# Kernel optimization log

Hardware: AMD Instinct MI355X
Metric: run time of the kernel (lower is better)

The kernel has to match this reference:

```python
import jax, jax.numpy as jnp
import numpy as np

N, C, D = 32768, 2048, 512

def setup_inputs() -> dict:
    key = jax.random.key(0)
    k1, k2, k3 = jax.random.split(key, 3)
    X = jax.random.normal(k1, (N, D), dtype=jnp.float32)
    muK = jax.random.normal(k2, (C, D), dtype=jnp.float32)
    # counts per class; zeros mark 'unvisited' classes exercising the masking path
    cK = jax.random.randint(k3, (C,), 0, 3).astype(jnp.float32)
    return {"X": X, "muK": muK, "cK": cK}

def reference(X, muK, cK):
    # find_dists(A=muK, B=X): dist[i, j] = sum_d (muK[j, d] - X[i, d])**2, scores = -dist
    # avoids materializing the N x C x D broadcast intermediate of the original).
    x2 = jnp.sum(X * X, axis=1, keepdims=True)          # (N, 1)
    m2 = jnp.sum(muK * muK, axis=1)                     # (C,)
    scores = -(x2 + m2[None, :] - 2.0 * (X @ muK.T))    # (N, C)
    # unvisited classes (cK == 0) get per-row min score minus 1
    min_col = jnp.min(scores, axis=1, keepdims=True) - 1.0  # (N, 1)
    scores = jnp.where((cK == 0.0)[None, :], min_col, scores)
    # predict(..., return_probas=True) as used in evaluate_
    return jax.nn.softmax(scores, axis=1)
```

## Files before the change

### kernel.cpp

```cpp
#include <hip/hip_runtime.h>
#include <cfloat>

#define N_ROWS 32768
#define N_CLS  2048
#define DIM    512

typedef __attribute__((ext_vector_type(8))) short short8;
typedef __attribute__((ext_vector_type(4))) short short4v;
typedef __attribute__((ext_vector_type(4))) float f32x4;

__device__ __forceinline__ unsigned f2bf_bits(float x) {
    union { float f; unsigned u; } a; a.f = x;
    return (a.u + 0x7fffu + ((a.u >> 16) & 1u)) >> 16;
}
__device__ __forceinline__ float bf_to_f(unsigned bits) {
    union { unsigned u; float f; } a; a.u = bits << 16;
    return a.f;
}
__device__ __forceinline__ void split_bf(float x, short &h, short &l) {
    unsigned hb = f2bf_bits(x);
    h = (short)hb;
    float r = x - bf_to_f(hb);
    l = (short)f2bf_bits(r);
}

__global__ __launch_bounds__(256) void split_kernel(const float* __restrict__ src,
                                                    short* __restrict__ hi,
                                                    short* __restrict__ lo) {
    int idx = blockIdx.x * 256 + threadIdx.x;
    float4 v = ((const float4*)src)[idx];
    short h0, h1, h2, h3, l0, l1, l2, l3;
    split_bf(v.x, h0, l0); split_bf(v.y, h1, l1);
    split_bf(v.z, h2, l2); split_bf(v.w, h3, l3);
    ((short4v*)hi)[idx] = (short4v){h0, h1, h2, h3};
    ((short4v*)lo)[idx] = (short4v){l0, l1, l2, l3};
}

__global__ __launch_bounds__(256) void m2_kernel(const float* __restrict__ muK,
                                                 float* __restrict__ m2) {
    const int j = blockIdx.x;
    const int t = threadIdx.x;
    const float* r = muK + (size_t)j * DIM;
    float a = r[t], b = r[t + 256];
    float s = a * a + b * b;
    for (int off = 32; off; off >>= 1) s += __shfl_xor(s, off);
    __shared__ float sw[4];
    if ((t & 63) == 0) sw[t >> 6] = s;
    __syncthreads();
    if (t == 0) m2[j] = sw[0] + sw[1] + sw[2] + sw[3];
}

#define GLDS16(g, l) __builtin_amdgcn_global_load_lds( \
    (const __attribute__((address_space(1))) unsigned int*)(g), \
    (__attribute__((address_space(3))) unsigned int*)(l), 16, 0, 0)

__global__ __launch_bounds__(256) void gemm_kernel(const short* __restrict__ Xh,
                                                   const short* __restrict__ Xl,
                                                   const short* __restrict__ Mh,
                                                   const short* __restrict__ Ml,
                                                   const float* __restrict__ m2,
                                                   float* __restrict__ S) {
    __shared__ __align__(16) short Ash[128 * 32];
    __shared__ __align__(16) short Asl[128 * 32];
    __shared__ __align__(16) short Bsh[128 * 32];
    __shared__ __align__(16) short Bsl[128 * 32];

    const int tid  = threadIdx.x;
    const int n0   = blockIdx.x * 128;
    const int m0   = blockIdx.y * 128;
    const int w    = tid >> 6;
    const int lane = tid & 63;
    const int wm   = (w >> 1) * 64;
    const int wn   = (w & 1) * 64;
    const int l16  = lane & 15;
    const int quad = lane >> 4;

    const int c0 = w * 128 + lane;
    const int c1 = c0 + 64;
    const size_t ga0 = (size_t)(m0 + (c0 >> 2)) * DIM + (size_t)(((c0 & 3) ^ ((c0 >> 3) & 3)) * 8);
    const size_t ga1 = (size_t)(m0 + (c1 >> 2)) * DIM + (size_t)(((c1 & 3) ^ ((c1 >> 3) & 3)) * 8);
    const size_t gb0 = (size_t)(n0 + (c0 >> 2)) * DIM + (size_t)(((c0 & 3) ^ ((c0 >> 3) & 3)) * 8);
    const size_t gb1 = (size_t)(n0 + (c1 >> 2)) * DIM + (size_t)(((c1 & 3) ^ ((c1 >> 3) & 3)) * 8);

    const int sw = (quad ^ ((l16 >> 1) & 3)) * 8;

    f32x4 acc[4][4];
#pragma unroll
    for (int mt = 0; mt < 4; ++mt)
#pragma unroll
        for (int nt = 0; nt < 4; ++nt)
            acc[mt][nt] = (f32x4){0.f, 0.f, 0.f, 0.f};

#pragma unroll 1
    for (int kt2 = 0; kt2 < 16; ++kt2) {
        const int kk = kt2 * 32;
        __syncthreads();
        GLDS16(Xh + ga0 + kk, &Ash[c0 * 8]);
        GLDS16(Xh + ga1 + kk, &Ash[c1 * 8]);
        GLDS16(Xl + ga0 + kk, &Asl[c0 * 8]);
        GLDS16(Xl + ga1 + kk, &Asl[c1 * 8]);
        GLDS16(Mh + gb0 + kk, &Bsh[c0 * 8]);
        GLDS16(Mh + gb1 + kk, &Bsh[c1 * 8]);
        GLDS16(Ml + gb0 + kk, &Bsl[c0 * 8]);
        GLDS16(Ml + gb1 + kk, &Bsl[c1 * 8]);
        __syncthreads();

        short8 ah[4], al[4];
#pragma unroll
        for (int mt = 0; mt < 4; ++mt) {
            const int ro = (wm + mt * 16 + l16) * 32 + sw;
            ah[mt] = *(const short8*)&Ash[ro];
            al[mt] = *(const short8*)&Asl[ro];
        }
#pragma unroll
        for (int nt = 0; nt < 4; ++nt) {
            const int ro = (wn + nt * 16 + l16) * 32 + sw;
            short8 bh = *(const short8*)&Bsh[ro];
            short8 bl = *(const short8*)&Bsl[ro];
#pragma unroll
            for (int mt = 0; mt < 4; ++mt)
                acc[mt][nt] = __builtin_amdgcn_mfma_f32_16x16x32_bf16(ah[mt], bh, acc[mt][nt], 0, 0, 0);
#pragma unroll
            for (int mt = 0; mt < 4; ++mt)
                acc[mt][nt] = __builtin_amdgcn_mfma_f32_16x16x32_bf16(ah[mt], bl, acc[mt][nt], 0, 0, 0);
#pragma unroll
            for (int mt = 0; mt < 4; ++mt)
                acc[mt][nt] = __builtin_amdgcn_mfma_f32_16x16x32_bf16(al[mt], bh, acc[mt][nt], 0, 0, 0);
        }
    }

#pragma unroll
    for (int nt = 0; nt < 4; ++nt) {
        int col = n0 + wn + nt * 16 + l16;
        float mm = m2[col];
#pragma unroll
        for (int mt = 0; mt < 4; ++mt) {
            int rbase = m0 + wm + mt * 16 + quad * 4;
#pragma unroll
            for (int r = 0; r < 4; ++r)
                S[(size_t)(rbase + r) * N_CLS + col] = 2.0f * acc[mt][nt][r] - mm;
        }
    }
}

#define LDR 40
__global__ __launch_bounds__(256) void gemm_fallback(const float* __restrict__ X,
                                                     const float* __restrict__ muK,
                                                     const float* __restrict__ m2,
                                                     float* __restrict__ S) {
    __shared__ __align__(16) short Ah[128 * LDR];
    __shared__ __align__(16) short Al[128 * LDR];
    __shared__ __align__(16) short Bh[128 * LDR];
    __shared__ __align__(16) short Bl[128 * LDR];
    const int tid  = threadIdx.x;
    const int n0   = blockIdx.x * 128;
    const int m0   = blockIdx.y * 128;
    const int w    = tid >> 6;
    const int lane = tid & 63;
    const int wm   = (w >> 1) * 64;
    const int wn   = (w & 1) * 64;
    const int l16  = lane & 15;
    const int quad = lane >> 4;
    f32x4 acc[4][4];
#pragma unroll
    for (int mt = 0; mt < 4; ++mt)
#pragma unroll
        for (int nt = 0; nt < 4; ++nt)
            acc[mt][nt] = (f32x4){0.f, 0.f, 0.f, 0.f};
    for (int kt = 0; kt < DIM; kt += 32) {
        __syncthreads();
#pragma unroll
        for (int i = 0; i < 4; ++i) {
            int idx = tid + 256 * i;
            int row = idx >> 3;
            int c4  = (idx & 7) * 4;
            float4 fa = *(const float4*)(X + (size_t)(m0 + row) * DIM + kt + c4);
            float4 fb = *(const float4*)(muK + (size_t)(n0 + row) * DIM + kt + c4);
            short h0, h1, h2, h3, l0, l1, l2, l3;
            split_bf(fa.x, h0, l0); split_bf(fa.y, h1, l1);
            split_bf(fa.z, h2, l2); split_bf(fa.w, h3, l3);
            *(short4v*)&Ah[row * LDR + c4] = (short4v){h0, h1, h2, h3};
            *(short4v*)&Al[row * LDR + c4] = (short4v){l0, l1, l2, l3};
            split_bf(fb.x, h0, l0); split_bf(fb.y, h1, l1);
            split_bf(fb.z, h2, l2); split_bf(fb.w, h3, l3);
            *(short4v*)&Bh[row * LDR + c4] = (short4v){h0, h1, h2, h3};
            *(short4v*)&Bl[row * LDR + c4] = (short4v){l0, l1, l2, l3};
        }
        __syncthreads();
        short8 ah[4], al[4];
#pragma unroll
        for (int mt = 0; mt < 4; ++mt) {
            int r = wm + mt * 16 + l16;
            ah[mt] = *(const short8*)&Ah[r * LDR + quad * 8];
            al[mt] = *(const short8*)&Al[r * LDR + quad * 8];
        }
#pragma unroll
        for (int nt = 0; nt < 4; ++nt) {
            int r = wn + nt * 16 + l16;
            short8 bh = *(const short8*)&Bh[r * LDR + quad * 8];
            short8 bl = *(const short8*)&Bl[r * LDR + quad * 8];
#pragma unroll
            for (int mt = 0; mt < 4; ++mt)
                acc[mt][nt] = __builtin_amdgcn_mfma_f32_16x16x32_bf16(ah[mt], bh, acc[mt][nt], 0, 0, 0);
#pragma unroll
            for (int mt = 0; mt < 4; ++mt)
                acc[mt][nt] = __builtin_amdgcn_mfma_f32_16x16x32_bf16(ah[mt], bl, acc[mt][nt], 0, 0, 0);
#pragma unroll
            for (int mt = 0; mt < 4; ++mt)
                acc[mt][nt] = __builtin_amdgcn_mfma_f32_16x16x32_bf16(al[mt], bh, acc[mt][nt], 0, 0, 0);
        }
    }
#pragma unroll
    for (int nt = 0; nt < 4; ++nt) {
        int col = n0 + wn + nt * 16 + l16;
        float mm = m2[col];
#pragma unroll
        for (int mt = 0; mt < 4; ++mt) {
            int rbase = m0 + wm + mt * 16 + quad * 4;
#pragma unroll
            for (int r = 0; r < 4; ++r)
                S[(size_t)(rbase + r) * N_CLS + col] = 2.0f * acc[mt][nt][r] - mm;
        }
    }
}

__device__ __forceinline__ void sm_load_row(float* S, int row, int lane, f32x4* v) {
    const f32x4* pi = (const f32x4*)(S + (size_t)row * N_CLS);
#pragma unroll
    for (int i = 0; i < 8; ++i) v[i] = pi[i * 64 + lane];
}

__device__ __forceinline__ void sm_compute_store(float* S, int row, int lane,
                                                 unsigned msk, f32x4* v) {
    float mn = FLT_MAX, mx = -FLT_MAX;
#pragma unroll
    for (int i = 0; i < 8; ++i) {
        f32x4 s = v[i];
        mn = fminf(mn, fminf(fminf(s.x, s.y), fminf(s.z, s.w)));
        if (!((msk >> (i * 4 + 0)) & 1u)) mx = fmaxf(mx, s.x);
        if (!((msk >> (i * 4 + 1)) & 1u)) mx = fmaxf(mx, s.y);
        if (!((msk >> (i * 4 + 2)) & 1u)) mx = fmaxf(mx, s.z);
        if (!((msk >> (i * 4 + 3)) & 1u)) mx = fmaxf(mx, s.w);
    }
    for (int off = 32; off; off >>= 1) {
        mn = fminf(mn, __shfl_xor(mn, off));
        mx = fmaxf(mx, __shfl_xor(mx, off));
    }
    if (mx == -FLT_MAX) mx = mn - 1.0f;
    const float fill = mn - 1.0f;

    float sum = 0.f;
#pragma unroll
    for (int i = 0; i < 8; ++i) {
        f32x4 s = v[i];
        s.x = __expf(((msk >> (i * 4 + 0)) & 1u ? fill : s.x) - mx);
        s.y = __expf(((msk >> (i * 4 + 1)) & 1u ? fill : s.y) - mx);
        s.z = __expf(((msk >> (i * 4 + 2)) & 1u ? fill : s.z) - mx);
        s.w = __expf(((msk >> (i * 4 + 3)) & 1u ? fill : s.w) - mx);
        sum += s.x + s.y + s.z + s.w;
        v[i] = s;
    }
    for (int off = 32; off; off >>= 1) sum += __shfl_xor(sum, off);
    const float inv = 1.0f / sum;
    f32x4* po = (f32x4*)(S + (size_t)row * N_CLS);
#pragma unroll
    for (int i = 0; i < 8; ++i) {
        f32x4 s = v[i] * inv;
        __builtin_nontemporal_store(s, &po[i * 64 + lane]);
    }
}

__global__ __launch_bounds__(256) void softmax_kernel(float* __restrict__ S,
                                                      const float* __restrict__ cK) {
    const int w    = threadIdx.x >> 6;
    const int lane = threadIdx.x & 63;
    const float4* ck4 = (const float4*)cK;

    unsigned msk = 0;
#pragma unroll
    for (int i = 0; i < 8; ++i) {
        float4 k = ck4[i * 64 + lane];
        if (k.x == 0.f) msk |= 1u << (i * 4 + 0);
        if (k.y == 0.f) msk |= 1u << (i * 4 + 1);
        if (k.z == 0.f) msk |= 1u << (i * 4 + 2);
        if (k.w == 0.f) msk |= 1u << (i * 4 + 3);
    }

    const int r0 = blockIdx.x * 16 + w * 4;
    f32x4 va[8], vb[8];

    sm_load_row(S, r0 + 0, lane, va);
    sm_load_row(S, r0 + 1, lane, vb);
    sm_compute_store(S, r0 + 0, lane, msk, va);
    sm_load_row(S, r0 + 2, lane, va);
    sm_compute_store(S, r0 + 1, lane, msk, vb);
    sm_load_row(S, r0 + 3, lane, vb);
    sm_compute_store(S, r0 + 2, lane, msk, va);
    sm_compute_store(S, r0 + 3, lane, msk, vb);
}

extern "C" void kernel_launch(void* const* d_in, const int* in_sizes, int n_in,
                              void* d_out, int out_size, void* d_ws, size_t ws_size,
                              hipStream_t stream) {
    const float* X   = (const float*)d_in[0];
    const float* muK = (const float*)d_in[1];
    const float* cK  = (const float*)d_in[2];
    float* out = (float*)d_out;

    const size_t XN = (size_t)N_ROWS * DIM;
    const size_t MN = (size_t)N_CLS * DIM;
    const size_t need = (2 * XN + 2 * MN) * sizeof(short) + N_CLS * sizeof(float);

    dim3 grid(N_CLS / 128, N_ROWS / 128);

    if (ws_size >= need) {
        short* Xh = (short*)d_ws;
        short* Xl = Xh + XN;
        short* Mh = Xl + XN;
        short* Ml = Mh + MN;
        float* m2 = (float*)(Ml + MN);
        split_kernel<<<(int)(XN / 4 / 256), 256, 0, stream>>>(X, Xh, Xl);
        split_kernel<<<(int)(MN / 4 / 256), 256, 0, stream>>>(muK, Mh, Ml);
        m2_kernel<<<N_CLS, 256, 0, stream>>>(muK, m2);
        gemm_kernel<<<grid, 256, 0, stream>>>(Xh, Xl, Mh, Ml, m2, out);
    } else {
        float* m2f = (float*)d_ws;
        m2_kernel<<<N_CLS, 256, 0, stream>>>(muK, m2f);
        gemm_fallback<<<grid, 256, 0, stream>>>(X, muK, m2f, out);
    }
    softmax_kernel<<<N_ROWS / 16, 256, 0, stream>>>(out, cK);
}
```

Baseline: 587.4 us.

## Double-buffer LDS tiles to overlap global loads with MFMA compute

The GEMM kernel's shared-memory tiles for the split bf16 hi/lo operands become two buffers each. The loads for the next K-slice are issued into the alternate buffer before the current slice's MFMAs run, and a sched_barrier keeps the compiler from reordering them. This replaces the two barriers per iteration with one at the end of the loop and hides load latency behind compute. In exchange, LDS per block doubles to 64KB, which can lower the number of resident blocks per CU.

After: 584.9 us. About the same (-0.4%).

```diff
diff --git a/kernel.cpp b/kernel.cpp
--- a/kernel.cpp
+++ b/kernel.cpp
@@ -60,10 +60,10 @@
                                                    const short* __restrict__ Ml,
                                                    const float* __restrict__ m2,
                                                    float* __restrict__ S) {
-    __shared__ __align__(16) short Ash[128 * 32];
-    __shared__ __align__(16) short Asl[128 * 32];
-    __shared__ __align__(16) short Bsh[128 * 32];
-    __shared__ __align__(16) short Bsl[128 * 32];
+    __shared__ __align__(16) short Ash[2][128 * 32];
+    __shared__ __align__(16) short Asl[2][128 * 32];
+    __shared__ __align__(16) short Bsh[2][128 * 32];
+    __shared__ __align__(16) short Bsl[2][128 * 32];
 
     const int tid  = threadIdx.x;
     const int n0   = blockIdx.x * 128;
@@ -84,6 +84,17 @@
 
     const int sw = (quad ^ ((l16 >> 1) & 3)) * 8;
 
+#define STAGE(B, KK) do { \
+        GLDS16(Xh + ga0 + (KK), &Ash[B][c0 * 8]); \
+        GLDS16(Xh + ga1 + (KK), &Ash[B][c1 * 8]); \
+        GLDS16(Xl + ga0 + (KK), &Asl[B][c0 * 8]); \
+        GLDS16(Xl + ga1 + (KK), &Asl[B][c1 * 8]); \
+        GLDS16(Mh + gb0 + (KK), &Bsh[B][c0 * 8]); \
+        GLDS16(Mh + gb1 + (KK), &Bsh[B][c1 * 8]); \
+        GLDS16(Ml + gb0 + (KK), &Bsl[B][c0 * 8]); \
+        GLDS16(Ml + gb1 + (KK), &Bsl[B][c1 * 8]); \
+    } while (0)
+
     f32x4 acc[4][4];
 #pragma unroll
     for (int mt = 0; mt < 4; ++mt)
@@ -91,32 +102,27 @@
         for (int nt = 0; nt < 4; ++nt)
             acc[mt][nt] = (f32x4){0.f, 0.f, 0.f, 0.f};
 
+    STAGE(0, 0);
+    __syncthreads();
+
 #pragma unroll 1
     for (int kt2 = 0; kt2 < 16; ++kt2) {
-        const int kk = kt2 * 32;
-        __syncthreads();
-        GLDS16(Xh + ga0 + kk, &Ash[c0 * 8]);
-        GLDS16(Xh + ga1 + kk, &Ash[c1 * 8]);
-        GLDS16(Xl + ga0 + kk, &Asl[c0 * 8]);
-        GLDS16(Xl + ga1 + kk, &Asl[c1 * 8]);
-        GLDS16(Mh + gb0 + kk, &Bsh[c0 * 8]);
-        GLDS16(Mh + gb1 + kk, &Bsh[c1 * 8]);
-        GLDS16(Ml + gb0 + kk, &Bsl[c0 * 8]);
-        GLDS16(Ml + gb1 + kk, &Bsl[c1 * 8]);
-        __syncthreads();
+        const int cur = kt2 & 1;
+        if (kt2 < 15) STAGE(cur ^ 1, kt2 * 32 + 32);
+        __builtin_amdgcn_sched_barrier(0);
 
         short8 ah[4], al[4];
 #pragma unroll
         for (int mt = 0; mt < 4; ++mt) {
             const int ro = (wm + mt * 16 + l16) * 32 + sw;
-            ah[mt] = *(const short8*)&Ash[ro];
-            al[mt] = *(const short8*)&Asl[ro];
+            ah[mt] = *(const short8*)&Ash[cur][ro];
+            al[mt] = *(const short8*)&Asl[cur][ro];
         }
 #pragma unroll
         for (int nt = 0; nt < 4; ++nt) {
             const int ro = (wn + nt * 16 + l16) * 32 + sw;
-            short8 bh = *(const short8*)&Bsh[ro];
-            short8 bl = *(const short8*)&Bsl[ro];
+            short8 bh = *(const short8*)&Bsh[cur][ro];
+            short8 bl = *(const short8*)&Bsl[cur][ro];
 #pragma unroll
             for (int mt = 0; mt < 4; ++mt)
                 acc[mt][nt] = __builtin_amdgcn_mfma_f32_16x16x32_bf16(ah[mt], bh, acc[mt][nt], 0, 0, 0);
@@ -127,7 +133,10 @@
             for (int mt = 0; mt < 4; ++mt)
                 acc[mt][nt] = __builtin_amdgcn_mfma_f32_16x16x32_bf16(al[mt], bh, acc[mt][nt], 0, 0, 0);
         }
-    }
+
+        __syncthreads();
+    }
+#undef STAGE
 
 #pragma unroll
     for (int nt = 0; nt < 4; ++nt) {
```
